# Performance work log

Measured on AMD Instinct MI355X. Metric: run time of the kernel, lower is better.

The kernel has to match this reference:

```python
import jax, jax.numpy as jnp
import numpy as np

NUM_EXPERT = 8
IN_FEAT = 1024
OUT_FEAT = 1024
N_TOKENS = 8192


def setup_inputs() -> dict:
    key = jax.random.key(0)
    k_inp, k_gate, k_w = jax.random.split(key, 3)
    inp = jax.random.normal(k_inp, (N_TOKENS, IN_FEAT), dtype=jnp.float32)
    gate = jax.random.randint(k_gate, (N_TOKENS,), 0, NUM_EXPERT, dtype=jnp.int32)
    # FMoELinear weight: [num_expert, out_feat, in_feat], kaiming-uniform-like init
    bound = 1.0 / np.sqrt(IN_FEAT)
    weight = jax.random.uniform(
        k_w, (NUM_EXPERT, OUT_FEAT, IN_FEAT), dtype=jnp.float32,
        minval=-bound, maxval=bound)
    return {"inp": inp, "gate": gate, "weight": weight}


def reference(inp, gate, weight):
    # out[i] = weight[gate[i]] @ inp[i]  (top-1 MoE dispatch + grouped GEMM + combine)
    # Loop over the small fixed expert set via scan; each step does a masked
    # dense GEMM so only tokens routed to expert e contribute.
    n, _ = inp.shape
    num_expert, out_feat, _ = weight.shape

    def body(acc, ew):
        e, w_e = ew  # w_e: [out_feat, in_feat]
        mask = (gate == e).astype(inp.dtype)[:, None]  # [n, 1]
        acc = acc + (inp * mask) @ w_e.T               # [n, out_feat]
        return acc, None

    init = jnp.zeros((n, out_feat), dtype=inp.dtype)
    out, _ = jax.lax.scan(body, init, (jnp.arange(num_expert), weight))
    return out
```

## Files before the change

kernel.cpp:

```cpp
#include <hip/hip_runtime.h>
#include <hip/hip_bf16.h>

#define N_TOKENS 8192
#define IN_FEAT 1024
#define OUT_FEAT 1024
#define NUM_EXPERT 8

#define BM 128
#define BN 128
#define BK 32

typedef __bf16 bf16x8 __attribute__((ext_vector_type(8)));
typedef float f32x4 __attribute__((ext_vector_type(4)));

__device__ __forceinline__ unsigned int rne16(float x) {
    union { float f; unsigned int u; } c;
    c.f = x;
    unsigned int u = c.u;
    u += 0x7fffu + ((u >> 16) & 1u);
    return u >> 16;
}
__device__ __forceinline__ unsigned int pk2(float x, float y) {
    return rne16(x) | (rne16(y) << 16);
}

__device__ __forceinline__ void load_lds16(const void* g, void* l) {
    __builtin_amdgcn_global_load_lds(
        (const __attribute__((address_space(1))) unsigned int*)g,
        (__attribute__((address_space(3))) unsigned int*)l,
        16, 0, 0);
}


__global__ __launch_bounds__(256) void moe_hist(const int* __restrict__ gate,
                                                int* __restrict__ cnt) {
    __shared__ int lc[NUM_EXPERT];
    const int t = threadIdx.x;
    if (t < NUM_EXPERT) lc[t] = 0;
    __syncthreads();
    int g = gate[blockIdx.x * 256 + t];
    atomicAdd(&lc[g], 1);
    __syncthreads();
    if (t < NUM_EXPERT) atomicAdd(&cnt[t], lc[t]);
}

__global__ void moe_scan(const int* __restrict__ cnt,
                         int* __restrict__ seg, int* __restrict__ cur) {
    int s = 0;
    #pragma unroll
    for (int e = 0; e < NUM_EXPERT; ++e) { seg[e] = s; cur[e] = s; s += cnt[e]; }
    seg[NUM_EXPERT] = s;
}

__global__ __launch_bounds__(256) void moe_scatter(const int* __restrict__ gate,
                                                   int* __restrict__ cur,
                                                   int* __restrict__ perm) {
    const int t = threadIdx.x;
    const int lane = t & 63;
    const unsigned long long lt = (lane == 0) ? 0ull : (~0ull >> (64 - lane));
    const int i = blockIdx.x * 256 + t;
    int g = gate[i];
    #pragma unroll
    for (int e = 0; e < NUM_EXPERT; ++e) {
        unsigned long long m = __ballot(g == e);
        if (g == e) {
            int rank = __popcll(m & lt);
            int leader = (int)__ffsll((unsigned long long)m) - 1;
            int p0 = 0;
            if (rank == 0) p0 = atomicAdd(&cur[e], __popcll(m));
            p0 = __shfl(p0, leader);
            perm[p0 + rank] = i;
        }
    }
}

__global__ __launch_bounds__(256) void moe_prep(const float* __restrict__ inp,
                                                const float* __restrict__ weight,
                                                unsigned int* __restrict__ A2,
                                                unsigned int* __restrict__ W2) {
    const int bid = blockIdx.x;
    const int t = threadIdx.x;
    const int wave = t >> 6, lane = t & 63;
    const float* src;
    unsigned int* dst;
    if (bid < 2048) {
        int row = bid * 4 + wave;
        src = inp + row * IN_FEAT;
        dst = A2 + row * (IN_FEAT / 2);
    } else {
        int row = (bid - 2048) * 4 + wave;
        src = weight + row * IN_FEAT;
        dst = W2 + row * (IN_FEAT / 2);
    }
    #pragma unroll
    for (int j = 0; j < 4; ++j) {
        float4 v = *(const float4*)(src + j * 256 + lane * 4);
        uint2 o;
        o.x = pk2(v.x, v.y);
        o.y = pk2(v.z, v.w);
        *(uint2*)(dst + j * 128 + lane * 2) = o;
    }
}

__global__ __launch_bounds__(256) void moe_gemm(
    const unsigned short* __restrict__ A2,
    const unsigned short* __restrict__ W2,
    const int* __restrict__ perm,
    const int* __restrict__ seg,
    float* __restrict__ out) {

    const int bid = blockIdx.x;
    const int ntile = bid >> 9;
    const int mtile = (bid >> 3) & 63;
    const int e = bid & 7;

    const int base = seg[e];
    const int cnt = seg[e + 1] - base;
    if (mtile * BM >= cnt) return;

    __shared__ unsigned short lA[BM * BK];
    __shared__ unsigned short lB[BN * BK];

    const int t = threadIdx.x;

    const int crow = t >> 2;
    const int p = (t & 3) ^ (crow & 3);
    int pr0 = base + mtile * BM + crow;
    int pr1 = pr0 + 64;
    pr0 = min(pr0, N_TOKENS - 1);
    pr1 = min(pr1, N_TOKENS - 1);
    const int tok0 = perm[pr0];
    const int tok1 = perm[pr1];
    const unsigned short* gA0 = A2 + tok0 * IN_FEAT + p * 8;
    const unsigned short* gA1 = A2 + tok1 * IN_FEAT + p * 8;
    const unsigned short* gB0 = W2 + e * (OUT_FEAT * IN_FEAT)
                                + (ntile * BN + crow) * IN_FEAT + p * 8;
    const unsigned short* gB1 = gB0 + 64 * IN_FEAT;
    unsigned short* dA0 = lA + t * 8;
    unsigned short* dA1 = lA + (t + 256) * 8;
    unsigned short* dB0 = lB + t * 8;
    unsigned short* dB1 = lB + (t + 256) * 8;

    const int wave = t >> 6;
    const int lane = t & 63;
    const int wm = (wave & 1) << 6;
    const int wn = (wave >> 1) << 6;
    const int l15 = lane & 15;
    const int quad = lane >> 4;
    const int qx = quad ^ (l15 & 3);
    const unsigned short* fA = lA + (wm + l15) * BK + qx * 8;
    const unsigned short* fB = lB + (wn + l15) * BK + qx * 8;

    f32x4 acc[4][4];
    #pragma unroll
    for (int i = 0; i < 4; ++i)
        #pragma unroll
        for (int j = 0; j < 4; ++j)
            acc[i][j] = (f32x4)0.0f;

    for (int k0 = 0; k0 < IN_FEAT; k0 += BK) {
        __syncthreads();
        load_lds16(gA0 + k0, dA0);
        load_lds16(gA1 + k0, dA1);
        load_lds16(gB0 + k0, dB0);
        load_lds16(gB1 + k0, dB1);
        __syncthreads();

        bf16x8 af[4], bq[4];
        #pragma unroll
        for (int i = 0; i < 4; ++i)
            af[i] = *(const bf16x8*)(fA + i * 16 * BK);
        #pragma unroll
        for (int j = 0; j < 4; ++j)
            bq[j] = *(const bf16x8*)(fB + j * 16 * BK);

        #pragma unroll
        for (int i = 0; i < 4; ++i)
            #pragma unroll
            for (int j = 0; j < 4; ++j)
                acc[i][j] = __builtin_amdgcn_mfma_f32_16x16x32_bf16(
                    af[i], bq[j], acc[i][j], 0, 0, 0);
    }

    #pragma unroll
    for (int mi = 0; mi < 4; ++mi) {
        #pragma unroll
        for (int r = 0; r < 4; ++r) {
            int row = wm + mi * 16 + quad * 4 + r;
            int grow = mtile * BM + row;
            if (grow < cnt) {
                int token = perm[base + grow];
                float* op = out + token * OUT_FEAT + ntile * BN + wn;
                #pragma unroll
                for (int ni = 0; ni < 4; ++ni)
                    op[ni * 16 + l15] = acc[mi][ni][r];
            }
        }
    }
}

#define FLDSW 20
__global__ __launch_bounds__(256, 4) void moe_gemm_fb(
    const float* __restrict__ inp,
    const float* __restrict__ weight,
    const int* __restrict__ perm,
    const int* __restrict__ seg,
    float* __restrict__ out) {

    const int bid = blockIdx.x;
    const int mtile = bid >> 7;
    const int e = (bid >> 4) & 7;
    const int ntile = bid & 15;

    const int base = seg[e];
    const int cnt = seg[e + 1] - base;
    if (mtile * 128 >= cnt) return;

    __shared__ unsigned int lA[128 * FLDSW];
    __shared__ unsigned int lB[64 * FLDSW];
    __shared__ int rowids[128];

    const int t = threadIdx.x;
    if (t < 128) {
        int r = mtile * 128 + t;
        rowids[t] = (r < cnt) ? perm[base + r] : -1;
    }
    __syncthreads();

    const int srow = t >> 1;
    const int scol = (t & 1) << 4;
    const int tokA = rowids[srow];
    const bool aval = (tokA >= 0);
    const float* aptr = inp + (aval ? tokA : 0) * IN_FEAT + scol;
    const int sdstA = srow * FLDSW + (scol >> 1);
    const int browB = t >> 2;
    const int bcol = (t & 3) << 3;
    const float* bptr = weight + e * (OUT_FEAT * IN_FEAT)
                        + (ntile * 64 + browB) * IN_FEAT + bcol;
    const int sdstB = browB * FLDSW + (bcol >> 1);

    const int wave = t >> 6;
    const int lane = t & 63;
    const int wm = (wave & 1) << 6;
    const int wn = (wave >> 1) << 5;
    const int l15 = lane & 15;
    const int quad = lane >> 4;

    f32x4 acc[4][2];
    #pragma unroll
    for (int i = 0; i < 4; ++i)
        #pragma unroll
        for (int j = 0; j < 2; ++j)
            acc[i][j] = (f32x4)0.0f;

    float4 ra[4], rb[2];
    {
        const float4* ap = (const float4*)aptr;
        const float4* bp = (const float4*)bptr;
        #pragma unroll
        for (int i = 0; i < 4; ++i) ra[i] = ap[i];
        #pragma unroll
        for (int i = 0; i < 2; ++i) rb[i] = bp[i];
    }

    for (int k0 = 0; k0 < IN_FEAT; k0 += 32) {
        unsigned int ua[8], ub[4];
        #pragma unroll
        for (int i = 0; i < 4; ++i) {
            ua[2 * i]     = pk2(ra[i].x, ra[i].y);
            ua[2 * i + 1] = pk2(ra[i].z, ra[i].w);
        }
        #pragma unroll
        for (int i = 0; i < 2; ++i) {
            ub[2 * i]     = pk2(rb[i].x, rb[i].y);
            ub[2 * i + 1] = pk2(rb[i].z, rb[i].w);
        }
        if (!aval) {
            #pragma unroll
            for (int i = 0; i < 8; ++i) ua[i] = 0u;
        }

        __syncthreads();
        *(uint4*)&lA[sdstA]     = make_uint4(ua[0], ua[1], ua[2], ua[3]);
        *(uint4*)&lA[sdstA + 4] = make_uint4(ua[4], ua[5], ua[6], ua[7]);
        *(uint4*)&lB[sdstB]     = make_uint4(ub[0], ub[1], ub[2], ub[3]);
        __syncthreads();

        if (k0 + 32 < IN_FEAT) {
            const float4* ap = (const float4*)(aptr + k0 + 32);
            const float4* bp = (const float4*)(bptr + k0 + 32);
            #pragma unroll
            for (int i = 0; i < 4; ++i) ra[i] = ap[i];
            #pragma unroll
            for (int i = 0; i < 2; ++i) rb[i] = bp[i];
        }

        bf16x8 af[4], bq[2];
        #pragma unroll
        for (int i = 0; i < 4; ++i)
            af[i] = *(const bf16x8*)&lA[(wm + i * 16 + l15) * FLDSW + (quad << 2)];
        #pragma unroll
        for (int j = 0; j < 2; ++j)
            bq[j] = *(const bf16x8*)&lB[(wn + j * 16 + l15) * FLDSW + (quad << 2)];

        #pragma unroll
        for (int i = 0; i < 4; ++i)
            #pragma unroll
            for (int j = 0; j < 2; ++j)
                acc[i][j] = __builtin_amdgcn_mfma_f32_16x16x32_bf16(
                    af[i], bq[j], acc[i][j], 0, 0, 0);
    }

    #pragma unroll
    for (int mi = 0; mi < 4; ++mi) {
        #pragma unroll
        for (int r = 0; r < 4; ++r) {
            int row = wm + mi * 16 + quad * 4 + r;
            int token = rowids[row];
            if (token >= 0) {
                float* op = out + token * OUT_FEAT + ntile * 64 + wn;
                #pragma unroll
                for (int ni = 0; ni < 2; ++ni)
                    op[ni * 16 + l15] = acc[mi][ni][r];
            }
        }
    }
}

extern "C" void kernel_launch(void* const* d_in, const int* in_sizes, int n_in,
                              void* d_out, int out_size, void* d_ws, size_t ws_size,
                              hipStream_t stream) {
    const float* inp = (const float*)d_in[0];
    const int* gate = (const int*)d_in[1];
    const float* weight = (const float*)d_in[2];
    float* out = (float*)d_out;

    int* perm = (int*)d_ws;
    int* seg = perm + N_TOKENS;
    int* cnt = seg + 16;
    int* cur = cnt + 8;

    hipMemsetAsync(cnt, 0, 16 * sizeof(int), stream);
    moe_hist<<<N_TOKENS / 256, 256, 0, stream>>>(gate, cnt);
    moe_scan<<<1, 1, 0, stream>>>(cnt, seg, cur);
    moe_scatter<<<N_TOKENS / 256, 256, 0, stream>>>(gate, cur, perm);

    const size_t need = 65536 + 2ull * N_TOKENS * IN_FEAT * 2;
    if (ws_size >= need) {
        unsigned int* A2 = (unsigned int*)((char*)d_ws + 65536);
        unsigned int* W2 = A2 + (N_TOKENS * IN_FEAT / 2);
        moe_prep<<<4096, 256, 0, stream>>>(inp, weight, A2, W2);
        const int grid = (OUT_FEAT / BN) * 512;
        moe_gemm<<<grid, 256, 0, stream>>>((const unsigned short*)A2,
                                           (const unsigned short*)W2,
                                           perm, seg, out);
    } else {
        moe_gemm_fb<<<8192, 256, 0, stream>>>(inp, weight, perm, seg, out);
    }
}
```

Measured before the change: 174.3 us.

## Compact tile list, pre-permute activations, and double-buffer LDS in MoE GEMM

The scan kernel now builds a compact list of (expert, row-base, rows) M-tiles, so the GEMM grid launches only about MAXT*8 blocks instead of many early-exiting ones. The prep kernel gathers input rows in permuted order, which makes A loads in the GEMM contiguous rather than indexed through perm. The K loop double-buffers LDS so the next 32-wide slice loads while MFMAs run on the current one, and launch bounds request 4 blocks per CU. In exchange it doubles LDS use and relies on a fixed MAXT bound on the tile count; launching more blocks than exist tiles is handled by an early exit.

```diff
diff --git a/kernel.cpp b/kernel.cpp
--- a/kernel.cpp
+++ b/kernel.cpp
@@ -9,6 +9,7 @@
 #define BM 128
 #define BN 128
 #define BK 32
+#define MAXT 71
 
 typedef __bf16 bf16x8 __attribute__((ext_vector_type(8)));
 typedef float f32x4 __attribute__((ext_vector_type(4)));
@@ -44,12 +45,22 @@
     if (t < NUM_EXPERT) atomicAdd(&cnt[t], lc[t]);
 }
 
-__global__ void moe_scan(const int* __restrict__ cnt,
-                         int* __restrict__ seg, int* __restrict__ cur) {
+__global__ void moe_scan(const int* __restrict__ cnt, int* __restrict__ seg,
+                         int* __restrict__ cur, int* __restrict__ tiles,
+                         int* __restrict__ ntiles) {
     int s = 0;
     #pragma unroll
     for (int e = 0; e < NUM_EXPERT; ++e) { seg[e] = s; cur[e] = s; s += cnt[e]; }
     seg[NUM_EXPERT] = s;
+    int T = 0;
+    for (int e = 0; e < NUM_EXPERT; ++e) {
+        int c = cnt[e], b = seg[e];
+        for (int mt = 0; mt * BM < c; ++mt) {
+            int rows = c - mt * BM; if (rows > BM) rows = BM;
+            tiles[T++] = (b + mt * BM) | (e << 13) | (rows << 16);
+        }
+    }
+    *ntiles = T;
 }
 
 __global__ __launch_bounds__(256) void moe_scatter(const int* __restrict__ gate,
@@ -76,6 +87,7 @@
 
 __global__ __launch_bounds__(256) void moe_prep(const float* __restrict__ inp,
                                                 const float* __restrict__ weight,
+                                                const int* __restrict__ perm,
                                                 unsigned int* __restrict__ A2,
                                                 unsigned int* __restrict__ W2) {
     const int bid = blockIdx.x;
@@ -85,7 +97,7 @@
     unsigned int* dst;
     if (bid < 2048) {
         int row = bid * 4 + wave;
-        src = inp + row * IN_FEAT;
+        src = inp + perm[row] * IN_FEAT;
         dst = A2 + row * (IN_FEAT / 2);
     } else {
         int row = (bid - 2048) * 4 + wave;
@@ -102,44 +114,44 @@
     }
 }
 
-__global__ __launch_bounds__(256) void moe_gemm(
+__global__ __launch_bounds__(256, 4) void moe_gemm(
     const unsigned short* __restrict__ A2,
     const unsigned short* __restrict__ W2,
     const int* __restrict__ perm,
-    const int* __restrict__ seg,
+    const int* __restrict__ tiles,
+    const int* __restrict__ ntiles,
     float* __restrict__ out) {
 
     const int bid = blockIdx.x;
-    const int ntile = bid >> 9;
-    const int mtile = (bid >> 3) & 63;
-    const int e = bid & 7;
-
-    const int base = seg[e];
-    const int cnt = seg[e + 1] - base;
-    if (mtile * BM >= cnt) return;
-
-    __shared__ unsigned short lA[BM * BK];
-    __shared__ unsigned short lB[BN * BK];
+    const int tIdx = bid >> 3;
+    const int ntile = bid & 7;
+    if (tIdx >= *ntiles) return;
+    const int tile = tiles[tIdx];
+    const int tbase = tile & 8191;
+    const int e = (tile >> 13) & 7;
+    const int rows = tile >> 16;
+
+    __shared__ unsigned short lA[2][BM * BK];
+    __shared__ unsigned short lB[2][BN * BK];
+    __shared__ int rowids[BM];
 
     const int t = threadIdx.x;
+    if (t < BM) {
+        int r = tbase + t;
+        rowids[t] = perm[r < N_TOKENS ? r : N_TOKENS - 1];
+    }
 
     const int crow = t >> 2;
     const int p = (t & 3) ^ (crow & 3);
-    int pr0 = base + mtile * BM + crow;
-    int pr1 = pr0 + 64;
-    pr0 = min(pr0, N_TOKENS - 1);
-    pr1 = min(pr1, N_TOKENS - 1);
-    const int tok0 = perm[pr0];
-    const int tok1 = perm[pr1];
-    const unsigned short* gA0 = A2 + tok0 * IN_FEAT + p * 8;
-    const unsigned short* gA1 = A2 + tok1 * IN_FEAT + p * 8;
+    int ar0 = tbase + crow;       if (ar0 > N_TOKENS - 1) ar0 = N_TOKENS - 1;
+    int ar1 = tbase + 64 + crow;  if (ar1 > N_TOKENS - 1) ar1 = N_TOKENS - 1;
+    const unsigned short* gA0 = A2 + ar0 * IN_FEAT + p * 8;
+    const unsigned short* gA1 = A2 + ar1 * IN_FEAT + p * 8;
     const unsigned short* gB0 = W2 + e * (OUT_FEAT * IN_FEAT)
                                 + (ntile * BN + crow) * IN_FEAT + p * 8;
     const unsigned short* gB1 = gB0 + 64 * IN_FEAT;
-    unsigned short* dA0 = lA + t * 8;
-    unsigned short* dA1 = lA + (t + 256) * 8;
-    unsigned short* dB0 = lB + t * 8;
-    unsigned short* dB1 = lB + (t + 256) * 8;
+    const int dofs = t * 8;
+    const int dofs2 = (t + 256) * 8;
 
     const int wave = t >> 6;
     const int lane = t & 63;
@@ -148,8 +160,8 @@
     const int l15 = lane & 15;
     const int quad = lane >> 4;
     const int qx = quad ^ (l15 & 3);
-    const unsigned short* fA = lA + (wm + l15) * BK + qx * 8;
-    const unsigned short* fB = lB + (wn + l15) * BK + qx * 8;
+    const int fofsA = (wm + l15) * BK + qx * 8;
+    const int fofsB = (wn + l15) * BK + qx * 8;
 
     f32x4 acc[4][4];
     #pragma unroll
@@ -158,28 +170,60 @@
         for (int j = 0; j < 4; ++j)
             acc[i][j] = (f32x4)0.0f;
 
-    for (int k0 = 0; k0 < IN_FEAT; k0 += BK) {
+    load_lds16(gA0, &lA[0][dofs]);
+    load_lds16(gA1, &lA[0][dofs2]);
+    load_lds16(gB0, &lB[0][dofs]);
+    load_lds16(gB1, &lB[0][dofs2]);
+
+    #pragma unroll 1
+    for (int kk = 0; kk < 16; ++kk) {
+        const int k0 = kk * 64;
+
         __syncthreads();
-        load_lds16(gA0 + k0, dA0);
-        load_lds16(gA1 + k0, dA1);
-        load_lds16(gB0 + k0, dB0);
-        load_lds16(gB1 + k0, dB1);
+        load_lds16(gA0 + k0 + 32, &lA[1][dofs]);
+        load_lds16(gA1 + k0 + 32, &lA[1][dofs2]);
+        load_lds16(gB0 + k0 + 32, &lB[1][dofs]);
+        load_lds16(gB1 + k0 + 32, &lB[1][dofs2]);
+
+        {
+            bf16x8 af[4], bq[4];
+            #pragma unroll
+            for (int i = 0; i < 4; ++i)
+                af[i] = *(const bf16x8*)&lA[0][fofsA + i * 16 * BK];
+            #pragma unroll
+            for (int j = 0; j < 4; ++j)
+                bq[j] = *(const bf16x8*)&lB[0][fofsB + j * 16 * BK];
+            #pragma unroll
+            for (int i = 0; i < 4; ++i)
+                #pragma unroll
+                for (int j = 0; j < 4; ++j)
+                    acc[i][j] = __builtin_amdgcn_mfma_f32_16x16x32_bf16(
+                        af[i], bq[j], acc[i][j], 0, 0, 0);
+        }
+
         __syncthreads();
-
-        bf16x8 af[4], bq[4];
-        #pragma unroll
-        for (int i = 0; i < 4; ++i)
-            af[i] = *(const bf16x8*)(fA + i * 16 * BK);
-        #pragma unroll
-        for (int j = 0; j < 4; ++j)
-            bq[j] = *(const bf16x8*)(fB + j * 16 * BK);
-
-        #pragma unroll
-        for (int i = 0; i < 4; ++i)
+        if (kk < 15) {
+            load_lds16(gA0 + k0 + 64, &lA[0][dofs]);
+            load_lds16(gA1 + k0 + 64, &lA[0][dofs2]);
+            load_lds16(gB0 + k0 + 64, &lB[0][dofs]);
+            load_lds16(gB1 + k0 + 64, &lB[0][dofs2]);
+        }
+
+        {
+            bf16x8 af[4], bq[4];
+            #pragma unroll
+            for (int i = 0; i < 4; ++i)
+                af[i] = *(const bf16x8*)&lA[1][fofsA + i * 16 * BK];
             #pragma unroll
             for (int j = 0; j < 4; ++j)
-                acc[i][j] = __builtin_amdgcn_mfma_f32_16x16x32_bf16(
-                    af[i], bq[j], acc[i][j], 0, 0, 0);
+                bq[j] = *(const bf16x8*)&lB[1][fofsB + j * 16 * BK];
+            #pragma unroll
+            for (int i = 0; i < 4; ++i)
+                #pragma unroll
+                for (int j = 0; j < 4; ++j)
+                    acc[i][j] = __builtin_amdgcn_mfma_f32_16x16x32_bf16(
+                        af[i], bq[j], acc[i][j], 0, 0, 0);
+        }
     }
 
     #pragma unroll
@@ -187,9 +231,8 @@
         #pragma unroll
         for (int r = 0; r < 4; ++r) {
             int row = wm + mi * 16 + quad * 4 + r;
-            int grow = mtile * BM + row;
-            if (grow < cnt) {
-                int token = perm[base + grow];
+            if (row < rows) {
+                int token = rowids[row];
                 float* op = out + token * OUT_FEAT + ntile * BN + wn;
                 #pragma unroll
                 for (int ni = 0; ni < 4; ++ni)
@@ -339,21 +382,22 @@
     int* seg = perm + N_TOKENS;
     int* cnt = seg + 16;
     int* cur = cnt + 8;
+    int* tiles = cur + 8;
+    int* ntiles = tiles + 96;
 
     hipMemsetAsync(cnt, 0, 16 * sizeof(int), stream);
     moe_hist<<<N_TOKENS / 256, 256, 0, stream>>>(gate, cnt);
-    moe_scan<<<1, 1, 0, stream>>>(cnt, seg, cur);
+    moe_scan<<<1, 1, 0, stream>>>(cnt, seg, cur, tiles, ntiles);
     moe_scatter<<<N_TOKENS / 256, 256, 0, stream>>>(gate, cur, perm);
 
     const size_t need = 65536 + 2ull * N_TOKENS * IN_FEAT * 2;
     if (ws_size >= need) {
         unsigned int* A2 = (unsigned int*)((char*)d_ws + 65536);
         unsigned int* W2 = A2 + (N_TOKENS * IN_FEAT / 2);
-        moe_prep<<<4096, 256, 0, stream>>>(inp, weight, A2, W2);
-        const int grid = (OUT_FEAT / BN) * 512;
-        moe_gemm<<<grid, 256, 0, stream>>>((const unsigned short*)A2,
-                                           (const unsigned short*)W2,
-                                           perm, seg, out);
+        moe_prep<<<4096, 256, 0, stream>>>(inp, weight, perm, A2, W2);
+        moe_gemm<<<MAXT * 8, 256, 0, stream>>>((const unsigned short*)A2,
+                                               (const unsigned short*)W2,
+                                               perm, tiles, ntiles, out);
     } else {
         moe_gemm_fb<<<8192, 256, 0, stream>>>(inp, weight, perm, seg, out);
     }
```

Measured after the change: 162.0 us. 7.0% less time.
